# Kernel optimization log

Hardware: AMD Instinct MI355X
Metric: run time of the kernel (lower is better)

The kernel has to match this reference:

```python
import jax, jax.numpy as jnp
import numpy as np

B, S, E, H = 4, 1024, 256, 12  # batch, seq, emb_dim, num_heads; per-head dim == E (module quirk)


def setup_inputs() -> dict:
    key = jax.random.key(0)
    ks = jax.random.split(key, 9)
    s = 0.02
    x = jax.random.normal(ks[0], (B, S, E), dtype=jnp.float32)
    # additive causal mask (the module's tril buffer is unused; mask arrives via attention_mask)
    causal = jnp.tril(jnp.ones((S, S), dtype=jnp.float32))
    attention_mask = ((1.0 - causal) * -10000.0)[None, None, :, :]
    Wq = jax.random.normal(ks[1], (E, E * H), dtype=jnp.float32) * s
    bq = jnp.zeros((E * H,), dtype=jnp.float32)
    Wk = jax.random.normal(ks[2], (E, E * H), dtype=jnp.float32) * s
    bk = jnp.zeros((E * H,), dtype=jnp.float32)
    Wv = jax.random.normal(ks[3], (E, E * H), dtype=jnp.float32) * s
    bv = jnp.zeros((E * H,), dtype=jnp.float32)
    Wfc = jax.random.normal(ks[4], (E * H, E), dtype=jnp.float32) * s
    bfc = jnp.zeros((E,), dtype=jnp.float32)
    return {"x": x, "attention_mask": attention_mask, "Wq": Wq, "bq": bq,
            "Wk": Wk, "bk": bk, "Wv": Wv, "bv": bv, "Wfc": Wfc, "bfc": bfc}


def _split_heads(t):
    # (B, S, H*E) -> (B, H, S, E)
    b, s, _ = t.shape
    return t.reshape(b, s, H, E).transpose(0, 2, 1, 3)


def reference(x, attention_mask, Wq, bq, Wk, bk, Wv, bv, Wfc, bfc):
    q = _split_heads(x @ Wq + bq)
    k = _split_heads(x @ Wk + bk)
    v = _split_heads(x @ Wv + bv)
    scale = 1.0 / jnp.sqrt(jnp.asarray(E, dtype=x.dtype))
    scores = jnp.einsum('bhqd,bhkd->bhqk', q, k) * scale + attention_mask
    probs = jax.nn.softmax(scores, axis=-1)  # dropout p=0 in eval reference
    ctx = jnp.einsum('bhqk,bhkd->bhqd', probs, v)
    merged = ctx.transpose(0, 2, 1, 3).reshape(x.shape[0], x.shape[1], H * E)
    return merged @ Wfc + bfc
```

## Files before the change

kernel.cpp:

```cpp
#include <hip/hip_runtime.h>

#define BATCH 4
#define SEQ   1024
#define EMB   256
#define NH    12
#define EH    3072
#define MROWS 4096

typedef __attribute__((ext_vector_type(8))) short bf16x8;
typedef __attribute__((ext_vector_type(4))) float f32x4;
typedef __attribute__((ext_vector_type(4))) short short4v;

__device__ __forceinline__ short f2bf(float f) {
  union { float f; unsigned u; } x; x.f = f;
  unsigned r = x.u + 0x7fffu + ((x.u >> 16) & 1u);
  return (short)(r >> 16);
}

__device__ __forceinline__ unsigned pack_trunc(float a, float b) {
  union { float f; unsigned u; } x, y;
  x.f = a; y.f = b;
  return (x.u >> 16) | (y.u & 0xffff0000u);
}

__device__ __forceinline__ void gload_lds16(const void* g, void* l) {
  __builtin_amdgcn_global_load_lds(
      (const __attribute__((address_space(1))) unsigned*)g,
      (__attribute__((address_space(3))) unsigned*)l, 16, 0, 0);
}

__global__ __launch_bounds__(256) void cast_x_kernel(const float* __restrict__ in,
                                                     short* __restrict__ out) {
  int i = (blockIdx.x * 256 + threadIdx.x) * 4;
  float4 v = *(const float4*)(in + i);
  short4v o;
  o[0] = f2bf(v.x); o[1] = f2bf(v.y); o[2] = f2bf(v.z); o[3] = f2bf(v.w);
  *(short4v*)(out + i) = o;
}

__global__ __launch_bounds__(256) void transpose_qkv_kernel(const float* __restrict__ Wq,
                                                            const float* __restrict__ Wk,
                                                            const float* __restrict__ Wv,
                                                            short* __restrict__ Wt) {
  __shared__ float tile[32][33];
  const float* W = blockIdx.z == 0 ? Wq : (blockIdx.z == 1 ? Wk : Wv);
  short* o = Wt + (size_t)blockIdx.z * EH * EMB;
  const int n0 = blockIdx.x * 32, k0 = blockIdx.y * 32;
  const int tx = threadIdx.x & 31, ty = threadIdx.x >> 5;
#pragma unroll
  for (int i = 0; i < 4; i++)
    tile[ty + 8 * i][tx] = W[(size_t)(k0 + ty + 8 * i) * EH + n0 + tx];
  __syncthreads();
#pragma unroll
  for (int i = 0; i < 4; i++) {
    int nr = ty + 8 * i;
    o[(size_t)(n0 + nr) * EMB + k0 + tx] = f2bf(tile[tx][nr]);
  }
}

__global__ __launch_bounds__(256) void transpose_cast_kernel(const float* __restrict__ W,
                                                             short* __restrict__ Wt,
                                                             int K, int N) {
  __shared__ float tile[32][33];
  const int n0 = blockIdx.x * 32, k0 = blockIdx.y * 32;
  const int tx = threadIdx.x & 31, ty = threadIdx.x >> 5;
#pragma unroll
  for (int i = 0; i < 4; i++)
    tile[ty + 8 * i][tx] = W[(size_t)(k0 + ty + 8 * i) * N + n0 + tx];
  __syncthreads();
#pragma unroll
  for (int i = 0; i < 4; i++) {
    int nr = ty + 8 * i;
    Wt[(size_t)(n0 + nr) * K + k0 + tx] = f2bf(tile[tx][nr]);
  }
}

__global__ __launch_bounds__(256) void qkv_gemm_kernel(const short* __restrict__ A,
                                                       const short* __restrict__ Bt,
                                                       const float* __restrict__ bq,
                                                       const float* __restrict__ bk,
                                                       const float* __restrict__ bv,
                                                       short* __restrict__ qout,
                                                       short* __restrict__ kout,
                                                       short* __restrict__ vout) {
  constexpr int BM = 128, BK = 64, K = EMB;
  __shared__ short As[2][BM * BK];
  __shared__ short Bs[2][BM * BK];
  const int tid = threadIdx.x;
  const int w = tid >> 6, lane = tid & 63;
  const int wm = w >> 1, wn = w & 1;
  const int l15 = lane & 15, l4 = lane >> 4;
  const int m0 = blockIdx.x * BM, n0 = blockIdx.y * BM;

  f32x4 acc[4][4] = {};

  int srow[4], scol[4];
#pragma unroll
  for (int i = 0; i < 4; i++) {
    const int idx = i * 256 + tid;
    const int row = idx >> 3, sp = idx & 7, sl = sp ^ (row & 7);
    srow[i] = row;
    scol[i] = sl * 8;
  }

#define QKV_STAGE(bu, k0)                                                        \
  {                                                                              \
    _Pragma("unroll") for (int i = 0; i < 4; i++) {                              \
      const int idx = i * 256 + tid;                                             \
      gload_lds16(A + (size_t)(m0 + srow[i]) * K + (k0) + scol[i],               \
                  (char*)&As[bu][0] + idx * 16);                                 \
      gload_lds16(Bt + (size_t)(n0 + srow[i]) * K + (k0) + scol[i],              \
                  (char*)&Bs[bu][0] + idx * 16);                                 \
    }                                                                            \
  }

  QKV_STAGE(0, 0);
  asm volatile("s_waitcnt vmcnt(0)" ::: "memory");
  __syncthreads();

  int bu = 0;
  for (int k0 = 0; k0 < K; k0 += BK) {
    if (k0 + BK < K) QKV_STAGE(bu ^ 1, k0 + BK);

#pragma unroll
    for (int kst = 0; kst < 2; kst++) {
      const int sp = (kst * 4 + l4) ^ (l15 & 7);
      bf16x8 af[4], bfr[4];
#pragma unroll
      for (int mt = 0; mt < 4; mt++)
        af[mt] = *(const bf16x8*)&As[bu][(wm * 64 + mt * 16 + l15) * 64 + sp * 8];
#pragma unroll
      for (int nt = 0; nt < 4; nt++)
        bfr[nt] = *(const bf16x8*)&Bs[bu][(wn * 64 + nt * 16 + l15) * 64 + sp * 8];
      __builtin_amdgcn_s_setprio(1);
#pragma unroll
      for (int mt = 0; mt < 4; mt++)
#pragma unroll
        for (int nt = 0; nt < 4; nt++)
          acc[mt][nt] = __builtin_amdgcn_mfma_f32_16x16x32_bf16(af[mt], bfr[nt], acc[mt][nt], 0, 0, 0);
      __builtin_amdgcn_s_setprio(0);
    }

    asm volatile("s_waitcnt vmcnt(0)" ::: "memory");
    __syncthreads();
    bu ^= 1;
  }

  const int region = n0 / 3072;
  const float* bias = region == 0 ? bq : (region == 1 ? bk : bv);
  const float kQScale = 0.09016844f;
#pragma unroll
  for (int nt = 0; nt < 4; nt++) {
    const int n = n0 + wn * 64 + nt * 16 + l15;
    const int col = n - region * 3072;
    const float bvv = bias[col];
#pragma unroll
    for (int mt = 0; mt < 4; mt++) {
      const int mrow = m0 + wm * 64 + mt * 16 + 4 * l4;
      f32x4 v = acc[mt][nt];
      if (region == 0) {
#pragma unroll
        for (int r = 0; r < 4; r++)
          qout[(size_t)(mrow + r) * EH + col] = f2bf((v[r] + bvv) * kQScale);
      } else if (region == 1) {
#pragma unroll
        for (int r = 0; r < 4; r++)
          kout[(size_t)(mrow + r) * EH + col] = f2bf(v[r] + bvv);
      } else {
        const int bb = mrow >> 10;
        const int s  = mrow & 1023;
        const int h  = col >> 8, d = col & 255;
        short4v o4;
        o4[0] = f2bf(v[0] + bvv); o4[1] = f2bf(v[1] + bvv);
        o4[2] = f2bf(v[2] + bvv); o4[3] = f2bf(v[3] + bvv);
        *(short4v*)&vout[((size_t)(bb * NH + h) * EMB + d) * SEQ + s] = o4;
      }
    }
  }
#undef QKV_STAGE
}

__global__ __launch_bounds__(256) void fc_gemm_kernel(const short* __restrict__ A,
                                                      const short* __restrict__ Bt,
                                                      const float* __restrict__ bias,
                                                      float* __restrict__ Cout,
                                                      int M, int N, int K) {
  constexpr int BM = 64, BK = 128;
  __shared__ short As[2][BM * BK];
  __shared__ short Bs[2][BM * BK];
  const int tid = threadIdx.x;
  const int w = tid >> 6, lane = tid & 63;
  const int wm = w >> 1, wn = w & 1;
  const int l15 = lane & 15, l4 = lane >> 4;
  const int m0 = blockIdx.x * BM, n0 = blockIdx.y * BM;

  f32x4 acc[2][2] = {};

  int srow[4], scol[4];
#pragma unroll
  for (int i = 0; i < 4; i++) {
    const int idx = i * 256 + tid;
    const int row = idx >> 4, sp = idx & 15, sl = sp ^ (row & 15);
    srow[i] = row;
    scol[i] = sl * 8;
  }

#define FC_STAGE(bu, k0)                                                         \
  {                                                                              \
    _Pragma("unroll") for (int i = 0; i < 4; i++) {                              \
      const int idx = i * 256 + tid;                                             \
      gload_lds16(A + (size_t)(m0 + srow[i]) * K + (k0) + scol[i],               \
                  (char*)&As[bu][0] + idx * 16);                                 \
      gload_lds16(Bt + (size_t)(n0 + srow[i]) * K + (k0) + scol[i],              \
                  (char*)&Bs[bu][0] + idx * 16);                                 \
    }                                                                            \
  }

  FC_STAGE(0, 0);
  asm volatile("s_waitcnt vmcnt(0)" ::: "memory");
  __syncthreads();

  int bu = 0;
  for (int k0 = 0; k0 < K; k0 += BK) {
    if (k0 + BK < K) FC_STAGE(bu ^ 1, k0 + BK);

#pragma unroll
    for (int kst = 0; kst < 4; kst++) {
      const int sp = (kst * 4 + l4) ^ l15;
      bf16x8 af[2], bfr[2];
#pragma unroll
      for (int mt = 0; mt < 2; mt++)
        af[mt] = *(const bf16x8*)&As[bu][(wm * 32 + mt * 16 + l15) * 128 + sp * 8];
#pragma unroll
      for (int nt = 0; nt < 2; nt++)
        bfr[nt] = *(const bf16x8*)&Bs[bu][(wn * 32 + nt * 16 + l15) * 128 + sp * 8];
      __builtin_amdgcn_s_setprio(1);
#pragma unroll
      for (int mt = 0; mt < 2; mt++)
#pragma unroll
        for (int nt = 0; nt < 2; nt++)
          acc[mt][nt] = __builtin_amdgcn_mfma_f32_16x16x32_bf16(af[mt], bfr[nt], acc[mt][nt], 0, 0, 0);
      __builtin_amdgcn_s_setprio(0);
    }

    asm volatile("s_waitcnt vmcnt(0)" ::: "memory");
    __syncthreads();
    bu ^= 1;
  }

#pragma unroll
  for (int nt = 0; nt < 2; nt++) {
    const int n = n0 + wn * 32 + nt * 16 + l15;
    const float bvv = bias[n];
#pragma unroll
    for (int mt = 0; mt < 2; mt++) {
      const int mrow = m0 + wm * 32 + mt * 16 + 4 * l4;
      f32x4 v = acc[mt][nt];
#pragma unroll
      for (int r = 0; r < 4; r++)
        Cout[(size_t)(mrow + r) * N + n] = v[r] + bvv;
    }
  }
#undef FC_STAGE
}

__global__ __launch_bounds__(512) void attn_kernel(const short* __restrict__ Q,
                                                   const short* __restrict__ Kg,
                                                   const short* __restrict__ Vt,
                                                   short* __restrict__ Ctx) {
  __shared__ short Ks[2][8192];
  __shared__ short Vs[2][8192];
  __shared__ short Ps[8][512];
  const int tid = threadIdx.x, w = tid >> 6, lane = tid & 63;
  const int l15 = lane & 15, l4 = lane >> 4;
  const int bh = blockIdx.x, b = bh / NH, h = bh % NH;
  const int qt = (gridDim.y - 1) - blockIdx.y;
  const int q0 = qt * 128;
  const int qw0 = q0 + w * 16;
  const int ntiles = 4 * qt + 4;

  const float kMaskL2 = -14426.95f;
  const float kThrL2  = 11.5f;

  const short* Kbase = Kg + (size_t)b * SEQ * EH + h * EMB;
  const short* Vbase = Vt + (size_t)bh * EMB * SEQ;

  int koff[2], voff[2];
#pragma unroll
  for (int i = 0; i < 2; i++) {
    const int idx = i * 512 + tid;
    {
      const int kv = (idx >> 3) & 31, sp = idx & 7, sl = sp ^ (kv & 7);
      koff[i] = kv * EH + (idx >> 8) * 64 + sl * 8;
    }
    {
      const int dp = idx >> 3, sp = idx & 7, sl = sp ^ (dp & 7);
      voff[i] = (dp * 2 + (sl >> 2)) * SEQ + (sl & 3) * 8;
    }
  }

  bf16x8 qf[8];
  {
    const short* qp = Q + (size_t)(b * SEQ + qw0 + l15) * EH + h * EMB + 8 * l4;
#pragma unroll
    for (int kst = 0; kst < 8; kst++) qf[kst] = *(const bf16x8*)(qp + 32 * kst);
  }

#pragma unroll
  for (int i = 0; i < 2; i++) {
    const int idx = i * 512 + tid;
    gload_lds16(Kbase + koff[i], (char*)&Ks[0][0] + idx * 16);
    gload_lds16(Vbase + voff[i], (char*)&Vs[0][0] + idx * 16);
  }
  asm volatile("s_waitcnt vmcnt(0)" ::: "memory");
  __syncthreads();

  f32x4 o[16] = {};
  float mst = -1e30f, lst = 0.f;

  int bu = 0;
  for (int t = 0; t < ntiles; t++) {
    const int kv0 = t * 32;

    if (t + 1 < ntiles) {
      const short* kp = Kbase + (size_t)(kv0 + 32) * EH;
      const short* vp = Vbase + kv0 + 32;
#pragma unroll
      for (int i = 0; i < 2; i++) {
        const int idx = i * 512 + tid;
        gload_lds16(kp + koff[i], (char*)&Ks[bu ^ 1][0] + idx * 16);
        gload_lds16(vp + voff[i], (char*)&Vs[bu ^ 1][0] + idx * 16);
      }
    }

    if (kv0 <= qw0 + 15) {
      f32x4 sf[2] = {};
      __builtin_amdgcn_s_setprio(1);
#pragma unroll
      for (int nt = 0; nt < 2; nt++)
#pragma unroll
        for (int kst = 0; kst < 8; kst++) {
          const int sp = (((kst & 1) << 2) + l4) ^ (l15 & 7);
          bf16x8 kf = *(const bf16x8*)&Ks[bu][(kst >> 1) * 2048 + (nt * 16 + l15) * 64 + sp * 8];
          sf[nt] = __builtin_amdgcn_mfma_f32_16x16x32_bf16(kf, qf[kst], sf[nt], 0, 0, 0);
        }
      __builtin_amdgcn_s_setprio(0);

      const bool maskt = (kv0 + 31 > qw0);
      float sval[2][4];
      float mxl = -1e30f;
#pragma unroll
      for (int nt = 0; nt < 2; nt++)
#pragma unroll
        for (int r = 0; r < 4; r++) {
          float s = sf[nt][r];
          if (maskt) {
            const int kv = kv0 + nt * 16 + 4 * l4 + r;
            s += (kv > qw0 + l15) ? kMaskL2 : 0.0f;
          }
          sval[nt][r] = s;
          mxl = fmaxf(mxl, s);
        }
      float mx = fmaxf(mxl, __shfl_xor(mxl, 16));
      mx = fmaxf(mx, __shfl_xor(mx, 32));
      const bool skipt = __all(mx <= mst + kThrL2);
      float mref, fsc;
      if (skipt) {
        fsc = 1.0f;
        mref = mst;
      } else {
        float mnew = fmaxf(mst, mx);
        fsc = exp2f(mst - mnew);
        mst = mnew;
        mref = mnew;
      }
      float pp[2][4];
      float lsum = 0.f;
#pragma unroll
      for (int nt = 0; nt < 2; nt++)
#pragma unroll
        for (int r = 0; r < 4; r++) {
          float e = exp2f(sval[nt][r] - mref);
          pp[nt][r] = e;
          lsum += e;
        }
      lst = lst * fsc + lsum;

      if (!skipt) {
        float fv[4];
#pragma unroll
        for (int r = 0; r < 4; r++)
          fv[r] = __shfl(fsc, (lane & 48) + 4 * (lane >> 4) + r);
#pragma unroll
        for (int nt = 0; nt < 16; nt++) {
          o[nt][0] *= fv[0]; o[nt][1] *= fv[1];
          o[nt][2] *= fv[2]; o[nt][3] *= fv[3];
        }
      }

#pragma unroll
      for (int nt = 0; nt < 2; nt++) {
        uint2 pk;
        pk.x = pack_trunc(pp[nt][0], pp[nt][1]);
        pk.y = pack_trunc(pp[nt][2], pp[nt][3]);
        const int col0 = nt * 16 + 4 * l4;
        const int pseg = (col0 >> 3) ^ ((l15 >> 1) & 3);
        *(uint2*)&Ps[w][l15 * 32 + pseg * 8 + (col0 & 7)] = pk;
      }

      const int aseg = l4 ^ ((l15 >> 1) & 3);
      bf16x8 af = *(const bf16x8*)&Ps[w][l15 * 32 + aseg * 8];
      const int vsp = ((l15 & 1) * 4 + l4) ^ (l15 >> 1);
      __builtin_amdgcn_s_setprio(1);
#pragma unroll
      for (int nt = 0; nt < 16; nt++) {
        const int dp = nt * 8 + (l15 >> 1);
        bf16x8 vf = *(const bf16x8*)&Vs[bu][dp * 64 + vsp * 8];
        o[nt] = __builtin_amdgcn_mfma_f32_16x16x32_bf16(af, vf, o[nt], 0, 0, 0);
      }
      __builtin_amdgcn_s_setprio(0);
    }

    asm volatile("s_waitcnt vmcnt(0)" ::: "memory");
    __syncthreads();
    bu ^= 1;
  }

  lst += __shfl_xor(lst, 16);
  lst += __shfl_xor(lst, 32);
  const float inv = 1.f / lst;
  float invv[4];
#pragma unroll
  for (int r = 0; r < 4; r++)
    invv[r] = __shfl(inv, (lane & 48) + 4 * (lane >> 4) + r);

  const int mrow = b * SEQ + qw0 + 4 * l4;
#pragma unroll
  for (int nt = 0; nt < 16; nt++) {
    const int d = h * EMB + nt * 16 + l15;
#pragma unroll
    for (int r = 0; r < 4; r++)
      Ctx[(size_t)(mrow + r) * EH + d] = f2bf(o[nt][r] * invv[r]);
  }
}

extern "C" void kernel_launch(void* const* d_in, const int* in_sizes, int n_in,
                              void* d_out, int out_size, void* d_ws, size_t ws_size,
                              hipStream_t stream) {
  const float* x   = (const float*)d_in[0];
  const float* Wq  = (const float*)d_in[2];
  const float* bq  = (const float*)d_in[3];
  const float* Wk  = (const float*)d_in[4];
  const float* bk  = (const float*)d_in[5];
  const float* Wv  = (const float*)d_in[6];
  const float* bv  = (const float*)d_in[7];
  const float* Wfc = (const float*)d_in[8];
  const float* bfc = (const float*)d_in[9];
  float* out = (float*)d_out;

  short* ws    = (short*)d_ws;
  short* xb    = ws;
  short* wqkvt = xb + 1048576;
  short* wfct  = wqkvt + 3 * 786432;
  short* q     = wfct + 786432;
  short* k     = q + 12582912;
  short* vt    = k + 12582912;
  short* ctx   = vt + 12582912;

  cast_x_kernel<<<1024, 256, 0, stream>>>(x, xb);
  transpose_qkv_kernel<<<dim3(EH / 32, EMB / 32, 3), 256, 0, stream>>>(Wq, Wk, Wv, wqkvt);
  transpose_cast_kernel<<<dim3(EMB / 32, EH / 32), 256, 0, stream>>>(Wfc, wfct, EH, EMB);

  qkv_gemm_kernel<<<dim3(MROWS / 128, 9216 / 128), 256, 0, stream>>>(
      xb, wqkvt, bq, bk, bv, q, k, vt);

  attn_kernel<<<dim3(BATCH * NH, SEQ / 128), 512, 0, stream>>>(q, k, vt, ctx);

  fc_gemm_kernel<<<dim3(MROWS / 64, EMB / 64), 256, 0, stream>>>(ctx, wfct, bfc, out, MROWS, EMB, EH);
}
```

Measured before the change: 151.0 us.

## Give each attention wave two 16-row query subtiles, halving block threads

The attention kernel now runs 4 waves of 64 threads per block instead of 8. Each wave processes 32 query rows as two 16-row subtiles, so every K and V fragment read from shared memory feeds two MFMAs. This cuts LDS read traffic per FLOP and spreads the per-block global-to-LDS copy over fewer threads. In exchange each wave holds twice the accumulator and Q registers, which could cause spills or lower occupancy, and causal skipping now works at 32-row granularity.

```diff
diff --git a/kernel.cpp b/kernel.cpp
--- a/kernel.cpp
+++ b/kernel.cpp
@@ -264,19 +264,19 @@
 #undef FC_STAGE
 }
 
-__global__ __launch_bounds__(512) void attn_kernel(const short* __restrict__ Q,
-                                                   const short* __restrict__ Kg,
-                                                   const short* __restrict__ Vt,
-                                                   short* __restrict__ Ctx) {
+__global__ __launch_bounds__(256, 2) void attn_kernel(const short* __restrict__ Q,
+                                                      const short* __restrict__ Kg,
+                                                      const short* __restrict__ Vt,
+                                                      short* __restrict__ Ctx) {
   __shared__ short Ks[2][8192];
   __shared__ short Vs[2][8192];
-  __shared__ short Ps[8][512];
+  __shared__ short Ps[4][2][512];
   const int tid = threadIdx.x, w = tid >> 6, lane = tid & 63;
   const int l15 = lane & 15, l4 = lane >> 4;
   const int bh = blockIdx.x, b = bh / NH, h = bh % NH;
   const int qt = (gridDim.y - 1) - blockIdx.y;
   const int q0 = qt * 128;
-  const int qw0 = q0 + w * 16;
+  const int qw0 = q0 + w * 32;
   const int ntiles = 4 * qt + 4;
 
   const float kMaskL2 = -14426.95f;
@@ -285,10 +285,10 @@
   const short* Kbase = Kg + (size_t)b * SEQ * EH + h * EMB;
   const short* Vbase = Vt + (size_t)bh * EMB * SEQ;
 
-  int koff[2], voff[2];
-#pragma unroll
-  for (int i = 0; i < 2; i++) {
-    const int idx = i * 512 + tid;
+  int koff[4], voff[4];
+#pragma unroll
+  for (int i = 0; i < 4; i++) {
+    const int idx = i * 256 + tid;
     {
       const int kv = (idx >> 3) & 31, sp = idx & 7, sl = sp ^ (kv & 7);
       koff[i] = kv * EH + (idx >> 8) * 64 + sl * 8;
@@ -299,24 +299,25 @@
     }
   }
 
-  bf16x8 qf[8];
-  {
-    const short* qp = Q + (size_t)(b * SEQ + qw0 + l15) * EH + h * EMB + 8 * l4;
-#pragma unroll
-    for (int kst = 0; kst < 8; kst++) qf[kst] = *(const bf16x8*)(qp + 32 * kst);
-  }
-
-#pragma unroll
-  for (int i = 0; i < 2; i++) {
-    const int idx = i * 512 + tid;
+  bf16x8 qf[2][8];
+#pragma unroll
+  for (int sub = 0; sub < 2; sub++) {
+    const short* qp = Q + (size_t)(b * SEQ + qw0 + sub * 16 + l15) * EH + h * EMB + 8 * l4;
+#pragma unroll
+    for (int kst = 0; kst < 8; kst++) qf[sub][kst] = *(const bf16x8*)(qp + 32 * kst);
+  }
+
+#pragma unroll
+  for (int i = 0; i < 4; i++) {
+    const int idx = i * 256 + tid;
     gload_lds16(Kbase + koff[i], (char*)&Ks[0][0] + idx * 16);
     gload_lds16(Vbase + voff[i], (char*)&Vs[0][0] + idx * 16);
   }
   asm volatile("s_waitcnt vmcnt(0)" ::: "memory");
   __syncthreads();
 
-  f32x4 o[16] = {};
-  float mst = -1e30f, lst = 0.f;
+  f32x4 o[2][16] = {};
+  float mst[2] = {-1e30f, -1e30f}, lst[2] = {0.f, 0.f};
 
   int bu = 0;
   for (int t = 0; t < ntiles; t++) {
@@ -326,15 +327,15 @@
       const short* kp = Kbase + (size_t)(kv0 + 32) * EH;
       const short* vp = Vbase + kv0 + 32;
 #pragma unroll
-      for (int i = 0; i < 2; i++) {
-        const int idx = i * 512 + tid;
+      for (int i = 0; i < 4; i++) {
+        const int idx = i * 256 + tid;
         gload_lds16(kp + koff[i], (char*)&Ks[bu ^ 1][0] + idx * 16);
         gload_lds16(vp + voff[i], (char*)&Vs[bu ^ 1][0] + idx * 16);
       }
     }
 
-    if (kv0 <= qw0 + 15) {
-      f32x4 sf[2] = {};
+    if (kv0 <= qw0 + 31) {
+      f32x4 sf[2][2] = {};
       __builtin_amdgcn_s_setprio(1);
 #pragma unroll
       for (int nt = 0; nt < 2; nt++)
@@ -342,81 +343,86 @@
         for (int kst = 0; kst < 8; kst++) {
           const int sp = (((kst & 1) << 2) + l4) ^ (l15 & 7);
           bf16x8 kf = *(const bf16x8*)&Ks[bu][(kst >> 1) * 2048 + (nt * 16 + l15) * 64 + sp * 8];
-          sf[nt] = __builtin_amdgcn_mfma_f32_16x16x32_bf16(kf, qf[kst], sf[nt], 0, 0, 0);
+          sf[0][nt] = __builtin_amdgcn_mfma_f32_16x16x32_bf16(kf, qf[0][kst], sf[0][nt], 0, 0, 0);
+          sf[1][nt] = __builtin_amdgcn_mfma_f32_16x16x32_bf16(kf, qf[1][kst], sf[1][nt], 0, 0, 0);
         }
       __builtin_amdgcn_s_setprio(0);
 
-      const bool maskt = (kv0 + 31 > qw0);
-      float sval[2][4];
-      float mxl = -1e30f;
-#pragma unroll
-      for (int nt = 0; nt < 2; nt++)
-#pragma unroll
-        for (int r = 0; r < 4; r++) {
-          float s = sf[nt][r];
-          if (maskt) {
+#pragma unroll
+      for (int sub = 0; sub < 2; sub++) {
+        const int qrow = qw0 + sub * 16 + l15;
+        const bool maskt = (kv0 + 31 > qrow) || (kv0 + 31 > qw0 + sub * 16);
+        float sval[2][4];
+        float mxl = -1e30f;
+#pragma unroll
+        for (int nt = 0; nt < 2; nt++)
+#pragma unroll
+          for (int r = 0; r < 4; r++) {
+            float s = sf[sub][nt][r];
             const int kv = kv0 + nt * 16 + 4 * l4 + r;
-            s += (kv > qw0 + l15) ? kMaskL2 : 0.0f;
+            s += (maskt && kv > qrow) ? kMaskL2 : 0.0f;
+            sval[nt][r] = s;
+            mxl = fmaxf(mxl, s);
           }
-          sval[nt][r] = s;
-          mxl = fmaxf(mxl, s);
+        float mx = fmaxf(mxl, __shfl_xor(mxl, 16));
+        mx = fmaxf(mx, __shfl_xor(mx, 32));
+        const bool skipt = __all(mx <= mst[sub] + kThrL2);
+        float mref, fsc;
+        if (skipt) {
+          fsc = 1.0f;
+          mref = mst[sub];
+        } else {
+          float mnew = fmaxf(mst[sub], mx);
+          fsc = exp2f(mst[sub] - mnew);
+          mst[sub] = mnew;
+          mref = mnew;
         }
-      float mx = fmaxf(mxl, __shfl_xor(mxl, 16));
-      mx = fmaxf(mx, __shfl_xor(mx, 32));
-      const bool skipt = __all(mx <= mst + kThrL2);
-      float mref, fsc;
-      if (skipt) {
-        fsc = 1.0f;
-        mref = mst;
-      } else {
-        float mnew = fmaxf(mst, mx);
-        fsc = exp2f(mst - mnew);
-        mst = mnew;
-        mref = mnew;
-      }
-      float pp[2][4];
-      float lsum = 0.f;
-#pragma unroll
-      for (int nt = 0; nt < 2; nt++)
-#pragma unroll
-        for (int r = 0; r < 4; r++) {
-          float e = exp2f(sval[nt][r] - mref);
-          pp[nt][r] = e;
-          lsum += e;
+        float pp[2][4];
+        float lsum = 0.f;
+#pragma unroll
+        for (int nt = 0; nt < 2; nt++)
+#pragma unroll
+          for (int r = 0; r < 4; r++) {
+            float e = exp2f(sval[nt][r] - mref);
+            pp[nt][r] = e;
+            lsum += e;
+          }
+        lst[sub] = lst[sub] * fsc + lsum;
+
+        if (!skipt) {
+          float fv[4];
+#pragma unroll
+          for (int r = 0; r < 4; r++)
+            fv[r] = __shfl(fsc, (lane & 48) + 4 * (lane >> 4) + r);
+#pragma unroll
+          for (int nt = 0; nt < 16; nt++) {
+            o[sub][nt][0] *= fv[0]; o[sub][nt][1] *= fv[1];
+            o[sub][nt][2] *= fv[2]; o[sub][nt][3] *= fv[3];
+          }
         }
-      lst = lst * fsc + lsum;
-
-      if (!skipt) {
-        float fv[4];
-#pragma unroll
-        for (int r = 0; r < 4; r++)
-          fv[r] = __shfl(fsc, (lane & 48) + 4 * (lane >> 4) + r);
-#pragma unroll
-        for (int nt = 0; nt < 16; nt++) {
-          o[nt][0] *= fv[0]; o[nt][1] *= fv[1];
-          o[nt][2] *= fv[2]; o[nt][3] *= fv[3];
+
+#pragma unroll
+        for (int nt = 0; nt < 2; nt++) {
+          uint2 pk;
+          pk.x = pack_trunc(pp[nt][0], pp[nt][1]);
+          pk.y = pack_trunc(pp[nt][2], pp[nt][3]);
+          const int col0 = nt * 16 + 4 * l4;
+          const int pseg = (col0 >> 3) ^ ((l15 >> 1) & 3);
+          *(uint2*)&Ps[w][sub][l15 * 32 + pseg * 8 + (col0 & 7)] = pk;
         }
       }
 
-#pragma unroll
-      for (int nt = 0; nt < 2; nt++) {
-        uint2 pk;
-        pk.x = pack_trunc(pp[nt][0], pp[nt][1]);
-        pk.y = pack_trunc(pp[nt][2], pp[nt][3]);
-        const int col0 = nt * 16 + 4 * l4;
-        const int pseg = (col0 >> 3) ^ ((l15 >> 1) & 3);
-        *(uint2*)&Ps[w][l15 * 32 + pseg * 8 + (col0 & 7)] = pk;
-      }
-
       const int aseg = l4 ^ ((l15 >> 1) & 3);
-      bf16x8 af = *(const bf16x8*)&Ps[w][l15 * 32 + aseg * 8];
+      bf16x8 af0 = *(const bf16x8*)&Ps[w][0][l15 * 32 + aseg * 8];
+      bf16x8 af1 = *(const bf16x8*)&Ps[w][1][l15 * 32 + aseg * 8];
       const int vsp = ((l15 & 1) * 4 + l4) ^ (l15 >> 1);
       __builtin_amdgcn_s_setprio(1);
 #pragma unroll
       for (int nt = 0; nt < 16; nt++) {
         const int dp = nt * 8 + (l15 >> 1);
         bf16x8 vf = *(const bf16x8*)&Vs[bu][dp * 64 + vsp * 8];
-        o[nt] = __builtin_amdgcn_mfma_f32_16x16x32_bf16(af, vf, o[nt], 0, 0, 0);
+        o[0][nt] = __builtin_amdgcn_mfma_f32_16x16x32_bf16(af0, vf, o[0][nt], 0, 0, 0);
+        o[1][nt] = __builtin_amdgcn_mfma_f32_16x16x32_bf16(af1, vf, o[1][nt], 0, 0, 0);
       }
       __builtin_amdgcn_s_setprio(0);
     }
@@ -426,21 +432,25 @@
     bu ^= 1;
   }
 
-  lst += __shfl_xor(lst, 16);
-  lst += __shfl_xor(lst, 32);
-  const float inv = 1.f / lst;
-  float invv[4];
-#pragma unroll
-  for (int r = 0; r < 4; r++)
-    invv[r] = __shfl(inv, (lane & 48) + 4 * (lane >> 4) + r);
-
-  const int mrow = b * SEQ + qw0 + 4 * l4;
-#pragma unroll
-  for (int nt = 0; nt < 16; nt++) {
-    const int d = h * EMB + nt * 16 + l15;
+#pragma unroll
+  for (int sub = 0; sub < 2; sub++) {
+    float ls = lst[sub];
+    ls += __shfl_xor(ls, 16);
+    ls += __shfl_xor(ls, 32);
+    const float inv = 1.f / ls;
+    float invv[4];
 #pragma unroll
     for (int r = 0; r < 4; r++)
-      Ctx[(size_t)(mrow + r) * EH + d] = f2bf(o[nt][r] * invv[r]);
+      invv[r] = __shfl(inv, (lane & 48) + 4 * (lane >> 4) + r);
+
+    const int mrow = b * SEQ + qw0 + sub * 16 + 4 * l4;
+#pragma unroll
+    for (int nt = 0; nt < 16; nt++) {
+      const int d = h * EMB + nt * 16 + l15;
+#pragma unroll
+      for (int r = 0; r < 4; r++)
+        Ctx[(size_t)(mrow + r) * EH + d] = f2bf(o[sub][nt][r] * invv[r]);
+    }
   }
 }
 
@@ -474,7 +484,7 @@
   qkv_gemm_kernel<<<dim3(MROWS / 128, 9216 / 128), 256, 0, stream>>>(
       xb, wqkvt, bq, bk, bv, q, k, vt);
 
-  attn_kernel<<<dim3(BATCH * NH, SEQ / 128), 512, 0, stream>>>(q, k, vt, ctx);
+  attn_kernel<<<dim3(BATCH * NH, SEQ / 128), 256, 0, stream>>>(q, k, vt, ctx);
 
   fc_gemm_kernel<<<dim3(MROWS / 64, EMB / 64), 256, 0, stream>>>(ctx, wfct, bfc, out, MROWS, EMB, EH);
 }
```

After: 170.1 us. 12.6% more time.

## Split-K the output projection GEMM with a separate reduction kernel

Applied to the files above, without the earlier changes.

The FC GEMM (K=3072) previously launched only 256 blocks, each walking the whole K dimension. It now splits K into 4 slices of 768, writing fp32 partials into the reused Q buffer. A new reduce kernel then sums the partials and adds the bias. This raises block count to fill the GPU, at the cost of extra partial-sum traffic (4x4096x256 floats) and one more launch.

```diff
diff --git a/kernel.cpp b/kernel.cpp
--- a/kernel.cpp
+++ b/kernel.cpp
@@ -180,12 +180,11 @@
 #undef QKV_STAGE
 }
 
-__global__ __launch_bounds__(256) void fc_gemm_kernel(const short* __restrict__ A,
-                                                      const short* __restrict__ Bt,
-                                                      const float* __restrict__ bias,
-                                                      float* __restrict__ Cout,
-                                                      int M, int N, int K) {
-  constexpr int BM = 64, BK = 128;
+__global__ __launch_bounds__(256) void fc_partial_kernel(const short* __restrict__ A,
+                                                         const short* __restrict__ Bt,
+                                                         float* __restrict__ Pout,
+                                                         int M, int N, int K) {
+  constexpr int BM = 64, BK = 128, KSL = 768;
   __shared__ short As[2][BM * BK];
   __shared__ short Bs[2][BM * BK];
   const int tid = threadIdx.x;
@@ -193,6 +192,8 @@
   const int wm = w >> 1, wn = w & 1;
   const int l15 = lane & 15, l4 = lane >> 4;
   const int m0 = blockIdx.x * BM, n0 = blockIdx.y * BM;
+  const int kbase = blockIdx.z * KSL;
+  float* P = Pout + (size_t)blockIdx.z * M * N;
 
   f32x4 acc[2][2] = {};
 
@@ -216,13 +217,13 @@
     }                                                                            \
   }
 
-  FC_STAGE(0, 0);
+  FC_STAGE(0, kbase);
   asm volatile("s_waitcnt vmcnt(0)" ::: "memory");
   __syncthreads();
 
   int bu = 0;
-  for (int k0 = 0; k0 < K; k0 += BK) {
-    if (k0 + BK < K) FC_STAGE(bu ^ 1, k0 + BK);
+  for (int k0 = kbase; k0 < kbase + KSL; k0 += BK) {
+    if (k0 + BK < kbase + KSL) FC_STAGE(bu ^ 1, k0 + BK);
 
 #pragma unroll
     for (int kst = 0; kst < 4; kst++) {
@@ -251,17 +252,30 @@
 #pragma unroll
   for (int nt = 0; nt < 2; nt++) {
     const int n = n0 + wn * 32 + nt * 16 + l15;
-    const float bvv = bias[n];
 #pragma unroll
     for (int mt = 0; mt < 2; mt++) {
       const int mrow = m0 + wm * 32 + mt * 16 + 4 * l4;
       f32x4 v = acc[mt][nt];
 #pragma unroll
       for (int r = 0; r < 4; r++)
-        Cout[(size_t)(mrow + r) * N + n] = v[r] + bvv;
+        P[(size_t)(mrow + r) * N + n] = v[r];
     }
   }
 #undef FC_STAGE
+}
+
+__global__ __launch_bounds__(256) void fc_reduce_kernel(const float* __restrict__ Pin,
+                                                        const float* __restrict__ bias,
+                                                        float* __restrict__ out) {
+  const int i4 = (blockIdx.x * 256 + threadIdx.x) * 4;
+  const int n = i4 & 255;
+  float4 s = *(const float4*)(bias + n);
+#pragma unroll
+  for (int ks = 0; ks < 4; ks++) {
+    float4 p = *(const float4*)(Pin + (size_t)ks * MROWS * EMB + i4);
+    s.x += p.x; s.y += p.y; s.z += p.z; s.w += p.w;
+  }
+  *(float4*)(out + i4) = s;
 }
 
 __global__ __launch_bounds__(512) void attn_kernel(const short* __restrict__ Q,
@@ -466,6 +480,7 @@
   short* k     = q + 12582912;
   short* vt    = k + 12582912;
   short* ctx   = vt + 12582912;
+  float* fcp   = (float*)q;
 
   cast_x_kernel<<<1024, 256, 0, stream>>>(x, xb);
   transpose_qkv_kernel<<<dim3(EH / 32, EMB / 32, 3), 256, 0, stream>>>(Wq, Wk, Wv, wqkvt);
@@ -476,5 +491,7 @@
 
   attn_kernel<<<dim3(BATCH * NH, SEQ / 128), 512, 0, stream>>>(q, k, vt, ctx);
 
-  fc_gemm_kernel<<<dim3(MROWS / 64, EMB / 64), 256, 0, stream>>>(ctx, wfct, bfc, out, MROWS, EMB, EH);
-}
+  fc_partial_kernel<<<dim3(MROWS / 64, EMB / 64, 4), 256, 0, stream>>>(
+      ctx, wfct, fcp, MROWS, EMB, EH);
+  fc_reduce_kernel<<<(MROWS * EMB / 4) / 256, 256, 0, stream>>>(fcp, bfc, out);
+}
```

Result: faster. 144.8 us (-4.1%).
